# Kernel tuning notes

Hardware: AMD Instinct MI355X
Metric: run time of the kernel (lower is better)

Reference implementation:

```python
import jax, jax.numpy as jnp
import numpy as np

D_MODEL = 512
N_HEADS = 8
HEAD_DIM = D_MODEL // N_HEADS
BATCH = 4
SEQ = 2048


def setup_inputs() -> dict:
    key = jax.random.key(0)
    ks = jax.random.split(key, 9)
    s = 1.0 / np.sqrt(D_MODEL)
    inp = {
        "x": jax.random.normal(ks[0], (BATCH, SEQ, D_MODEL), dtype=jnp.float32),
        "wq": jax.random.uniform(ks[1], (D_MODEL, D_MODEL), jnp.float32, -s, s),
        "bq": jax.random.uniform(ks[2], (D_MODEL,), jnp.float32, -s, s),
        "wk": jax.random.uniform(ks[3], (D_MODEL, D_MODEL), jnp.float32, -s, s),
        "bk": jax.random.uniform(ks[4], (D_MODEL,), jnp.float32, -s, s),
        "wv": jax.random.uniform(ks[5], (D_MODEL, D_MODEL), jnp.float32, -s, s),
        "bv": jax.random.uniform(ks[6], (D_MODEL,), jnp.float32, -s, s),
        "wo": jax.random.uniform(ks[7], (D_MODEL, D_MODEL), jnp.float32, -s, s),
        "bo": jax.random.uniform(ks[8], (D_MODEL,), jnp.float32, -s, s),
    }
    return inp


def reference(x, wq, bq, wk, bk, wv, bv, wo, bo):
    B, S, D = x.shape
    H, Hd = N_HEADS, HEAD_DIM
    # projections (torch Linear: y = x @ W^T + b; here weights stored as [in, out])
    q = (x @ wq + bq).reshape(B, S, H, Hd).transpose(0, 2, 1, 3)  # [B,H,S,Hd]
    k = (x @ wk + bk).reshape(B, S, H, Hd).transpose(0, 2, 1, 3)
    v = (x @ wv + bv).reshape(B, S, H, Hd).transpose(0, 2, 1, 3)
    scores = jnp.einsum("bhqd,bhkd->bhqk", q, k) / jnp.sqrt(jnp.float32(Hd))
    attn = jax.nn.softmax(scores, axis=-1)
    o = jnp.einsum("bhqk,bhkd->bhqd", attn, v)  # [B,H,S,Hd]
    o = o.transpose(0, 2, 1, 3).reshape(B, S, D)
    return o @ wo + bo
```

## Files before the change

kernel.cpp:

```cpp
#include <hip/hip_runtime.h>
#include <math.h>

#define DM   512
#define SEQL 2048
#define NB   4
#define NH   8
#define HD   64

typedef _Float16 f16;
typedef _Float16 f16x4 __attribute__((ext_vector_type(4)));
typedef _Float16 f16x8 __attribute__((ext_vector_type(8)));
typedef float    f32x4 __attribute__((ext_vector_type(4)));

#define QSCALE 0.1803368801f
#define SOFTMAX_SHIFT 4.328085123f

typedef const __attribute__((address_space(1))) void* gp1_t;
typedef __attribute__((address_space(3))) void* lp3_t;
__device__ __forceinline__ void glds16(const void* g, void* l) {
    __builtin_amdgcn_global_load_lds((gp1_t)g, (lp3_t)l, 16, 0, 0);
}

__device__ __forceinline__ float fast_exp2(float x) {
#if __has_builtin(__builtin_amdgcn_exp2f)
    return __builtin_amdgcn_exp2f(x);
#else
    return exp2f(x);
#endif
}

__global__ __launch_bounds__(256) void prep_kernel(
    const float* __restrict__ x, f16* __restrict__ xh,
    const float* __restrict__ w0, const float* __restrict__ w1,
    const float* __restrict__ w2, const float* __restrict__ w3,
    f16* __restrict__ o0, f16* __restrict__ o1,
    f16* __restrict__ o2, f16* __restrict__ o3)
{
    __shared__ f16 t[64][72];
    const int bx = blockIdx.x;
    if (bx < 2048) {
        int i = (bx * 256 + threadIdx.x) * 8;
        float4 a = *(const float4*)&x[i];
        float4 b = *(const float4*)&x[i + 4];
        f16x8 h;
        h[0] = (f16)a.x; h[1] = (f16)a.y; h[2] = (f16)a.z; h[3] = (f16)a.w;
        h[4] = (f16)b.x; h[5] = (f16)b.y; h[6] = (f16)b.z; h[7] = (f16)b.w;
        *(f16x8*)&xh[i] = h;
        return;
    }
    const int idx  = bx - 2048;
    const int wsel = idx >> 6, tile = idx & 63;
    const float* w; f16* o;
    switch (wsel) {
        case 0:  w = w0; o = o0; break;
        case 1:  w = w1; o = o1; break;
        case 2:  w = w2; o = o2; break;
        default: w = w3; o = o3; break;
    }
    const int n0 = (tile & 7) * 64, k0 = (tile >> 3) * 64;
    const int tx = threadIdx.x & 63, tg = threadIdx.x >> 6;
    #pragma unroll
    for (int r = 0; r < 16; ++r) {
        int kl = tg * 16 + r;
        t[tx][kl] = (f16)w[(size_t)(k0 + kl) * DM + n0 + tx];
    }
    __syncthreads();
    #pragma unroll
    for (int r = 0; r < 16; ++r) {
        int nl = tg * 16 + r;
        o[(size_t)(n0 + nl) * DM + k0 + tx] = t[nl][tx];
    }
}

__global__ __launch_bounds__(256) void gemm_qkv(
    const f16* __restrict__ A, const f16* __restrict__ Wt,
    const float* __restrict__ bq, const float* __restrict__ bk,
    const float* __restrict__ bv,
    f16* __restrict__ qh, f16* __restrict__ kh, f16* __restrict__ vth)
{
    __shared__ f16 As[128 * 32];
    __shared__ f16 Bs[128 * 32];

    const int tid  = threadIdx.x;
    const int lane = tid & 63, wave = tid >> 6;
    const int quad = lane >> 4, l15 = lane & 15;
    const int wm = wave >> 1, wn = wave & 1;
    const int n0 = blockIdx.x * 128, m0 = blockIdx.y * 128;

    const int srow = wave * 32 + (lane >> 2);
    const int sk   = (lane & 3) * 8;

    f32x4 acc[4][4] = {};

    for (int k0 = 0; k0 < DM; k0 += 32) {
        glds16(&A [(size_t)(m0 + srow)      * DM + k0 + sk], &As[(wave * 32)      * 32]);
        glds16(&A [(size_t)(m0 + srow + 16) * DM + k0 + sk], &As[(wave * 32 + 16) * 32]);
        glds16(&Wt[(size_t)(n0 + srow)      * DM + k0 + sk], &Bs[(wave * 32)      * 32]);
        glds16(&Wt[(size_t)(n0 + srow + 16) * DM + k0 + sk], &Bs[(wave * 32 + 16) * 32]);
        __syncthreads();

        f16x8 af[4], bf[4];
        #pragma unroll
        for (int mt = 0; mt < 4; ++mt)
            af[mt] = *(f16x8*)&As[(wm * 64 + mt * 16 + l15) * 32 + quad * 8];
        #pragma unroll
        for (int nt = 0; nt < 4; ++nt)
            bf[nt] = *(f16x8*)&Bs[(wn * 64 + nt * 16 + l15) * 32 + quad * 8];
        #pragma unroll
        for (int mt = 0; mt < 4; ++mt)
            #pragma unroll
            for (int nt = 0; nt < 4; ++nt)
                acc[mt][nt] = __builtin_amdgcn_mfma_f32_16x16x32_f16(
                    af[mt], bf[nt], acc[mt][nt], 0, 0, 0);
        __syncthreads();
    }

    #pragma unroll
    for (int nt = 0; nt < 4; ++nt) {
        const int n   = n0 + wn * 64 + nt * 16 + l15;
        const int seg = n >> 9, nn = n & 511;
        const int h = nn >> 6, hd = nn & 63;
        const float bias = (seg == 0 ? bq : seg == 1 ? bk : bv)[nn];
        if (seg < 2) {
            f16* op = seg == 0 ? qh : kh;
            #pragma unroll
            for (int mt = 0; mt < 4; ++mt)
                #pragma unroll
                for (int rr = 0; rr < 4; ++rr) {
                    const int m = m0 + wm * 64 + mt * 16 + quad * 4 + rr;
                    const int bb = m >> 11, s = m & 2047;
                    op[(((size_t)(bb * NH + h) * SEQL + s) << 6) + hd] =
                        (f16)(acc[mt][nt][rr] + bias);
                }
        } else {
            #pragma unroll
            for (int mt = 0; mt < 4; ++mt) {
                const int mb = m0 + wm * 64 + mt * 16 + quad * 4;
                const int bb = mb >> 11, s = mb & 2047;
                f16x4 pk;
                #pragma unroll
                for (int rr = 0; rr < 4; ++rr) pk[rr] = (f16)(acc[mt][nt][rr] + bias);
                *(f16x4*)&vth[(((size_t)(bb * NH + h) * HD + hd) << 11) + s] = pk;
            }
        }
    }
}

__global__ __launch_bounds__(256) void gemm_out(
    const f16* __restrict__ A, const f16* __restrict__ Wt,
    const float* __restrict__ bias, float* __restrict__ out)
{
    __shared__ f16 As[128 * 32];
    __shared__ f16 Bs[128 * 32];

    const int tid  = threadIdx.x;
    const int lane = tid & 63, wave = tid >> 6;
    const int quad = lane >> 4, l15 = lane & 15;
    const int wm = wave >> 1, wn = wave & 1;
    const int n0 = blockIdx.x * 128, m0 = blockIdx.y * 128;

    const int srow = wave * 32 + (lane >> 2);
    const int sk   = (lane & 3) * 8;

    f32x4 acc[4][4] = {};

    for (int k0 = 0; k0 < DM; k0 += 32) {
        glds16(&A [(size_t)(m0 + srow)      * DM + k0 + sk], &As[(wave * 32)      * 32]);
        glds16(&A [(size_t)(m0 + srow + 16) * DM + k0 + sk], &As[(wave * 32 + 16) * 32]);
        glds16(&Wt[(size_t)(n0 + srow)      * DM + k0 + sk], &Bs[(wave * 32)      * 32]);
        glds16(&Wt[(size_t)(n0 + srow + 16) * DM + k0 + sk], &Bs[(wave * 32 + 16) * 32]);
        __syncthreads();

        f16x8 af[4], bf[4];
        #pragma unroll
        for (int mt = 0; mt < 4; ++mt)
            af[mt] = *(f16x8*)&As[(wm * 64 + mt * 16 + l15) * 32 + quad * 8];
        #pragma unroll
        for (int nt = 0; nt < 4; ++nt)
            bf[nt] = *(f16x8*)&Bs[(wn * 64 + nt * 16 + l15) * 32 + quad * 8];
        #pragma unroll
        for (int mt = 0; mt < 4; ++mt)
            #pragma unroll
            for (int nt = 0; nt < 4; ++nt)
                acc[mt][nt] = __builtin_amdgcn_mfma_f32_16x16x32_f16(
                    af[mt], bf[nt], acc[mt][nt], 0, 0, 0);
        __syncthreads();
    }

    #pragma unroll
    for (int nt = 0; nt < 4; ++nt) {
        const int n = n0 + wn * 64 + nt * 16 + l15;
        const float bv = bias[n];
        #pragma unroll
        for (int mt = 0; mt < 4; ++mt)
            #pragma unroll
            for (int rr = 0; rr < 4; ++rr) {
                const int m = m0 + wm * 64 + mt * 16 + quad * 4 + rr;
                out[(size_t)m * DM + n] = acc[mt][nt][rr] + bv;
            }
    }
}

__global__ __launch_bounds__(512) void flash_attn_mfma(
    const f16* __restrict__ Q, const f16* __restrict__ K,
    const f16* __restrict__ Vt, f16* __restrict__ O)
{
    __shared__ __align__(16) char smem[73728];
    f16*   Ks = (f16*)smem;
    f16*   Vs = (f16*)(smem + 18432);
    f16*   Ps = (f16*)(smem + 35840);
    float* Lx = (float*)(smem + 72704);
    float* cs = (float*)smem;

    const int tid  = threadIdx.x;
    const int lane = tid & 63, wave = tid >> 6;
    const int quad = lane >> 4, l15 = lane & 15;
    const int g  = wave >> 2;
    const int qg = wave & 3;
    const int bh = blockIdx.y, q0 = blockIdx.x * 128;
    const int b = bh >> 3, h = bh & 7;
    f16* Pw = Ps + wave * (32 * 72);

    const f16* Qb = Q  + (size_t)bh * SEQL * HD;
    const f16* Kb = K  + (size_t)bh * SEQL * HD;
    const f16* Vb = Vt + (size_t)bh * HD * SEQL;

    f16x8 qf[2][2];
    #pragma unroll
    for (int mq = 0; mq < 2; ++mq)
        #pragma unroll
        for (int ks = 0; ks < 2; ++ks) {
            qf[mq][ks] = *(const f16x8*)
                &Qb[(size_t)(q0 + qg * 32 + mq * 16 + l15) * HD + ks * 32 + quad * 8];
            #pragma unroll
            for (int j = 0; j < 8; ++j) qf[mq][ks][j] *= (f16)QSCALE;
        }

    const int krow = tid >> 3, kch = (tid & 7) * 8;
    const int vrow = tid >> 4, vch = (tid & 15) * 8;

    f16x8 kreg[2], vreg[2];
    #pragma unroll
    for (int r = 0; r < 2; ++r) {
        kreg[r] = *(const f16x8*)&Kb[(size_t)(krow + r * 64) * HD + kch];
        vreg[r] = *(const f16x8*)&Vb[(size_t)(vrow + r * 32) * SEQL + vch];
    }

    f32x4 o_acc[2][4] = {};
    float l_acc[2] = {0.f, 0.f};

    for (int kt = 0; kt < SEQL / 128; ++kt) {
        __syncthreads();
        #pragma unroll
        for (int r = 0; r < 2; ++r) {
            *(f16x8*)&Ks[(krow + r * 64) * 72 + kch]  = kreg[r];
            *(f16x8*)&Vs[(vrow + r * 32) * 136 + vch] = vreg[r];
        }
        __syncthreads();
        if (kt < SEQL / 128 - 1) {
            const int kb2 = (kt + 1) * 128;
            #pragma unroll
            for (int r = 0; r < 2; ++r) {
                kreg[r] = *(const f16x8*)&Kb[(size_t)(kb2 + krow + r * 64) * HD + kch];
                vreg[r] = *(const f16x8*)&Vb[(size_t)(vrow + r * 32) * SEQL + kb2 + vch];
            }
        }

        f32x4 sc[4][2];
        #pragma unroll
        for (int mk = 0; mk < 4; ++mk)
            #pragma unroll
            for (int mq = 0; mq < 2; ++mq)
                sc[mk][mq] = (f32x4){-SOFTMAX_SHIFT, -SOFTMAX_SHIFT,
                                     -SOFTMAX_SHIFT, -SOFTMAX_SHIFT};
        #pragma unroll
        for (int ks = 0; ks < 2; ++ks) {
            #pragma unroll
            for (int mk = 0; mk < 4; ++mk) {
                f16x8 af = *(f16x8*)&Ks[(g * 64 + mk * 16 + l15) * 72 + ks * 32 + quad * 8];
                #pragma unroll
                for (int mq = 0; mq < 2; ++mq)
                    sc[mk][mq] = __builtin_amdgcn_mfma_f32_16x16x32_f16(
                        af, qf[mq][ks], sc[mk][mq], 0, 0, 0);
            }
        }

        #pragma unroll
        for (int mk = 0; mk < 4; ++mk)
            #pragma unroll
            for (int mq = 0; mq < 2; ++mq) {
                float p0 = fast_exp2(sc[mk][mq][0]);
                float p1 = fast_exp2(sc[mk][mq][1]);
                float p2 = fast_exp2(sc[mk][mq][2]);
                float p3 = fast_exp2(sc[mk][mq][3]);
                l_acc[mq] += (p0 + p1) + (p2 + p3);
                f16x4 pk;
                pk[0] = (f16)p0; pk[1] = (f16)p1;
                pk[2] = (f16)p2; pk[3] = (f16)p3;
                *(f16x4*)&Pw[(mq * 16 + l15) * 72 + mk * 16 + quad * 4] = pk;
            }

        #pragma unroll
        for (int kc = 0; kc < 2; ++kc) {
            f16x8 pa0 = *(f16x8*)&Pw[(l15)      * 72 + kc * 32 + quad * 8];
            f16x8 pa1 = *(f16x8*)&Pw[(16 + l15) * 72 + kc * 32 + quad * 8];
            #pragma unroll
            for (int nt = 0; nt < 4; ++nt) {
                f16x8 vb = *(f16x8*)&Vs[(nt * 16 + l15) * 136 + g * 64 + kc * 32 + quad * 8];
                o_acc[0][nt] = __builtin_amdgcn_mfma_f32_16x16x32_f16(
                    pa0, vb, o_acc[0][nt], 0, 0, 0);
                o_acc[1][nt] = __builtin_amdgcn_mfma_f32_16x16x32_f16(
                    pa1, vb, o_acc[1][nt], 0, 0, 0);
            }
        }
    }

    #pragma unroll
    for (int mq = 0; mq < 2; ++mq) {
        float rs = l_acc[mq];
        rs += __shfl_xor(rs, 16);
        rs += __shfl_xor(rs, 32);
        l_acc[mq] = rs;
    }

    __syncthreads();
    if (quad == 0) {
        Lx[wave * 32 + l15]      = l_acc[0];
        Lx[wave * 32 + 16 + l15] = l_acc[1];
    }
    if (g == 1) {
        #pragma unroll
        for (int mq = 0; mq < 2; ++mq)
            #pragma unroll
            for (int r = 0; r < 4; ++r) {
                const int ql = mq * 16 + quad * 4 + r;
                #pragma unroll
                for (int nt = 0; nt < 4; ++nt)
                    cs[(qg * 32 + ql) * 68 + nt * 16 + l15] = o_acc[mq][nt][r];
            }
    }
    __syncthreads();
    if (g == 0) {
        #pragma unroll
        for (int mq = 0; mq < 2; ++mq)
            #pragma unroll
            for (int r = 0; r < 4; ++r) {
                const int ql = mq * 16 + quad * 4 + r;
                const float inv = 1.0f / (Lx[qg * 32 + ql] + Lx[(4 + qg) * 32 + ql]);
                const int s = q0 + qg * 32 + ql;
                #pragma unroll
                for (int nt = 0; nt < 4; ++nt) {
                    float ov = o_acc[mq][nt][r] + cs[(qg * 32 + ql) * 68 + nt * 16 + l15];
                    O[((size_t)(b * SEQL + s)) * DM + h * HD + nt * 16 + l15] =
                        (f16)(ov * inv);
                }
            }
    }
}

extern "C" void kernel_launch(void* const* d_in, const int* in_sizes, int n_in,
                              void* d_out, int out_size, void* d_ws, size_t ws_size,
                              hipStream_t stream) {
    const float* x  = (const float*)d_in[0];
    const float* wq = (const float*)d_in[1];
    const float* bq = (const float*)d_in[2];
    const float* wk = (const float*)d_in[3];
    const float* bk = (const float*)d_in[4];
    const float* wv = (const float*)d_in[5];
    const float* bv = (const float*)d_in[6];
    const float* wo = (const float*)d_in[7];
    const float* bo = (const float*)d_in[8];

    const size_t NE = (size_t)NB * SEQL * DM;
    const size_t WE = (size_t)DM * DM;
    f16* xh    = (f16*)d_ws;
    f16* wqkvt = xh + NE;
    f16* wot   = wqkvt + 3 * WE;
    f16* qh    = wot + WE;
    f16* kh    = qh + NE;
    f16* vth   = kh + NE;
    f16* oh    = vth + NE;

    prep_kernel<<<2304, 256, 0, stream>>>(
        x, xh, wq, wk, wv, wo,
        wqkvt, wqkvt + WE, wqkvt + 2 * WE, wot);

    gemm_qkv<<<dim3(12, 64), 256, 0, stream>>>(
        xh, wqkvt, bq, bk, bv, qh, kh, vth);

    flash_attn_mfma<<<dim3(SEQL / 128, NB * NH), 512, 0, stream>>>(qh, kh, vth, oh);

    gemm_out<<<dim3(4, 64), 256, 0, stream>>>(oh, wot, bo, (float*)d_out);
}
```

Measured before the change: 176.2 us.

## Vectorize GEMM epilogues via operand swap, retile out-proj, MFMA row sums in attention

The QKV GEMM swaps its MFMA operands for Q/K blocks so each lane holds four consecutive head-dim values, which lets the epilogue write packed f16x4 stores and load the bias as a vector. The output GEMM moves to 64x128 tiles with twice as many blocks, also swaps operands, and writes f32x4 vector stores. In flash attention the softmax row sums come from an extra MFMA against a ones vector instead of scalar adds and shuffles, and P is packed with cvt_pkrtz. The exp2 helper now calls exp2f, which may be slower than the raw builtin, and the extra MFMAs add matrix-unit work.

```diff
diff --git a/kernel.cpp b/kernel.cpp
--- a/kernel.cpp
+++ b/kernel.cpp
@@ -8,6 +8,7 @@
 #define HD   64
 
 typedef _Float16 f16;
+typedef __fp16   fp16x2 __attribute__((ext_vector_type(2)));
 typedef _Float16 f16x4 __attribute__((ext_vector_type(4)));
 typedef _Float16 f16x8 __attribute__((ext_vector_type(8)));
 typedef float    f32x4 __attribute__((ext_vector_type(4)));
@@ -21,13 +22,7 @@
     __builtin_amdgcn_global_load_lds((gp1_t)g, (lp3_t)l, 16, 0, 0);
 }
 
-__device__ __forceinline__ float fast_exp2(float x) {
-#if __has_builtin(__builtin_amdgcn_exp2f)
-    return __builtin_amdgcn_exp2f(x);
-#else
-    return exp2f(x);
-#endif
-}
+__device__ __forceinline__ float fast_exp2(float x) { return exp2f(x); }
 
 __global__ __launch_bounds__(256) void prep_kernel(
     const float* __restrict__ x, f16* __restrict__ xh,
@@ -86,6 +81,7 @@
     const int quad = lane >> 4, l15 = lane & 15;
     const int wm = wave >> 1, wn = wave & 1;
     const int n0 = blockIdx.x * 128, m0 = blockIdx.y * 128;
+    const bool qk = (blockIdx.x < 8);
 
     const int srow = wave * 32 + (lane >> 2);
     const int sk   = (lane & 3) * 8;
@@ -101,45 +97,63 @@
 
         f16x8 af[4], bf[4];
         #pragma unroll
-        for (int mt = 0; mt < 4; ++mt)
-            af[mt] = *(f16x8*)&As[(wm * 64 + mt * 16 + l15) * 32 + quad * 8];
-        #pragma unroll
-        for (int nt = 0; nt < 4; ++nt)
-            bf[nt] = *(f16x8*)&Bs[(wn * 64 + nt * 16 + l15) * 32 + quad * 8];
-        #pragma unroll
-        for (int mt = 0; mt < 4; ++mt)
-            #pragma unroll
-            for (int nt = 0; nt < 4; ++nt)
-                acc[mt][nt] = __builtin_amdgcn_mfma_f32_16x16x32_f16(
-                    af[mt], bf[nt], acc[mt][nt], 0, 0, 0);
-        __syncthreads();
-    }
-
-    #pragma unroll
-    for (int nt = 0; nt < 4; ++nt) {
-        const int n   = n0 + wn * 64 + nt * 16 + l15;
-        const int seg = n >> 9, nn = n & 511;
-        const int h = nn >> 6, hd = nn & 63;
-        const float bias = (seg == 0 ? bq : seg == 1 ? bk : bv)[nn];
-        if (seg < 2) {
-            f16* op = seg == 0 ? qh : kh;
-            #pragma unroll
-            for (int mt = 0; mt < 4; ++mt)
-                #pragma unroll
-                for (int rr = 0; rr < 4; ++rr) {
-                    const int m = m0 + wm * 64 + mt * 16 + quad * 4 + rr;
-                    const int bb = m >> 11, s = m & 2047;
-                    op[(((size_t)(bb * NH + h) * SEQL + s) << 6) + hd] =
-                        (f16)(acc[mt][nt][rr] + bias);
-                }
+        for (int i = 0; i < 4; ++i)
+            af[i] = *(f16x8*)&As[(wm * 64 + i * 16 + l15) * 32 + quad * 8];
+        #pragma unroll
+        for (int i = 0; i < 4; ++i)
+            bf[i] = *(f16x8*)&Bs[(wn * 64 + i * 16 + l15) * 32 + quad * 8];
+        if (qk) {
+            #pragma unroll
+            for (int i = 0; i < 4; ++i)
+                #pragma unroll
+                for (int j = 0; j < 4; ++j)
+                    acc[i][j] = __builtin_amdgcn_mfma_f32_16x16x32_f16(
+                        bf[i], af[j], acc[i][j], 0, 0, 0);
         } else {
             #pragma unroll
-            for (int mt = 0; mt < 4; ++mt) {
-                const int mb = m0 + wm * 64 + mt * 16 + quad * 4;
+            for (int i = 0; i < 4; ++i)
+                #pragma unroll
+                for (int j = 0; j < 4; ++j)
+                    acc[i][j] = __builtin_amdgcn_mfma_f32_16x16x32_f16(
+                        af[i], bf[j], acc[i][j], 0, 0, 0);
+        }
+        __syncthreads();
+    }
+
+    const int nwave = n0 + wn * 64;
+    const int seg   = nwave >> 9;
+    const int nn0   = nwave & 511;
+    const int h     = nn0 >> 6;
+
+    if (qk) {
+        f16* op = seg == 0 ? qh : kh;
+        const float* bp = seg == 0 ? bq : bk;
+        #pragma unroll
+        for (int i = 0; i < 4; ++i) {
+            const int hd = i * 16 + quad * 4;
+            f32x4 bv4 = *(const f32x4*)&bp[nn0 + hd];
+            #pragma unroll
+            for (int j = 0; j < 4; ++j) {
+                const int m = m0 + wm * 64 + j * 16 + l15;
+                const int bb = m >> 11, s = m & 2047;
+                f16x4 pk;
+                #pragma unroll
+                for (int rr = 0; rr < 4; ++rr) pk[rr] = (f16)(acc[i][j][rr] + bv4[rr]);
+                *(f16x4*)&op[(((size_t)(bb * NH + h) * SEQL + s) << 6) + hd] = pk;
+            }
+        }
+    } else {
+        #pragma unroll
+        for (int j = 0; j < 4; ++j) {
+            const int hd = j * 16 + l15;
+            const float bias = bv[nn0 + hd];
+            #pragma unroll
+            for (int i = 0; i < 4; ++i) {
+                const int mb = m0 + wm * 64 + i * 16 + quad * 4;
                 const int bb = mb >> 11, s = mb & 2047;
                 f16x4 pk;
                 #pragma unroll
-                for (int rr = 0; rr < 4; ++rr) pk[rr] = (f16)(acc[mt][nt][rr] + bias);
+                for (int rr = 0; rr < 4; ++rr) pk[rr] = (f16)(acc[i][j][rr] + bias);
                 *(f16x4*)&vth[(((size_t)(bb * NH + h) * HD + hd) << 11) + s] = pk;
             }
         }
@@ -150,54 +164,53 @@
     const f16* __restrict__ A, const f16* __restrict__ Wt,
     const float* __restrict__ bias, float* __restrict__ out)
 {
-    __shared__ f16 As[128 * 32];
+    __shared__ f16 As[64 * 32];
     __shared__ f16 Bs[128 * 32];
 
     const int tid  = threadIdx.x;
     const int lane = tid & 63, wave = tid >> 6;
     const int quad = lane >> 4, l15 = lane & 15;
-    const int wm = wave >> 1, wn = wave & 1;
-    const int n0 = blockIdx.x * 128, m0 = blockIdx.y * 128;
-
-    const int srow = wave * 32 + (lane >> 2);
-    const int sk   = (lane & 3) * 8;
-
-    f32x4 acc[4][4] = {};
+    const int wn = wave >> 1, wm = wave & 1;
+    const int n0 = blockIdx.x * 128, m0 = blockIdx.y * 64;
+
+    const int srowA = wave * 16 + (lane >> 2);
+    const int srowB = wave * 32 + (lane >> 2);
+    const int sk    = (lane & 3) * 8;
+
+    f32x4 acc[4][2] = {};
 
     for (int k0 = 0; k0 < DM; k0 += 32) {
-        glds16(&A [(size_t)(m0 + srow)      * DM + k0 + sk], &As[(wave * 32)      * 32]);
-        glds16(&A [(size_t)(m0 + srow + 16) * DM + k0 + sk], &As[(wave * 32 + 16) * 32]);
-        glds16(&Wt[(size_t)(n0 + srow)      * DM + k0 + sk], &Bs[(wave * 32)      * 32]);
-        glds16(&Wt[(size_t)(n0 + srow + 16) * DM + k0 + sk], &Bs[(wave * 32 + 16) * 32]);
-        __syncthreads();
-
-        f16x8 af[4], bf[4];
-        #pragma unroll
-        for (int mt = 0; mt < 4; ++mt)
-            af[mt] = *(f16x8*)&As[(wm * 64 + mt * 16 + l15) * 32 + quad * 8];
-        #pragma unroll
-        for (int nt = 0; nt < 4; ++nt)
-            bf[nt] = *(f16x8*)&Bs[(wn * 64 + nt * 16 + l15) * 32 + quad * 8];
-        #pragma unroll
-        for (int mt = 0; mt < 4; ++mt)
-            #pragma unroll
-            for (int nt = 0; nt < 4; ++nt)
-                acc[mt][nt] = __builtin_amdgcn_mfma_f32_16x16x32_f16(
-                    af[mt], bf[nt], acc[mt][nt], 0, 0, 0);
-        __syncthreads();
-    }
-
-    #pragma unroll
-    for (int nt = 0; nt < 4; ++nt) {
-        const int n = n0 + wn * 64 + nt * 16 + l15;
-        const float bv = bias[n];
-        #pragma unroll
-        for (int mt = 0; mt < 4; ++mt)
-            #pragma unroll
-            for (int rr = 0; rr < 4; ++rr) {
-                const int m = m0 + wm * 64 + mt * 16 + quad * 4 + rr;
-                out[(size_t)m * DM + n] = acc[mt][nt][rr] + bv;
-            }
+        glds16(&A [(size_t)(m0 + srowA)      * DM + k0 + sk], &As[(wave * 16)      * 32]);
+        glds16(&Wt[(size_t)(n0 + srowB)      * DM + k0 + sk], &Bs[(wave * 32)      * 32]);
+        glds16(&Wt[(size_t)(n0 + srowB + 16) * DM + k0 + sk], &Bs[(wave * 32 + 16) * 32]);
+        __syncthreads();
+
+        f16x8 af[4], bf[2];
+        #pragma unroll
+        for (int i = 0; i < 4; ++i)
+            af[i] = *(f16x8*)&Bs[(wn * 64 + i * 16 + l15) * 32 + quad * 8];
+        #pragma unroll
+        for (int j = 0; j < 2; ++j)
+            bf[j] = *(f16x8*)&As[(wm * 32 + j * 16 + l15) * 32 + quad * 8];
+        #pragma unroll
+        for (int i = 0; i < 4; ++i)
+            #pragma unroll
+            for (int j = 0; j < 2; ++j)
+                acc[i][j] = __builtin_amdgcn_mfma_f32_16x16x32_f16(
+                    af[i], bf[j], acc[i][j], 0, 0, 0);
+        __syncthreads();
+    }
+
+    #pragma unroll
+    for (int i = 0; i < 4; ++i) {
+        const int nb = n0 + wn * 64 + i * 16 + quad * 4;
+        f32x4 bv4 = *(const f32x4*)&bias[nb];
+        #pragma unroll
+        for (int j = 0; j < 2; ++j) {
+            const int m = m0 + wm * 32 + j * 16 + l15;
+            f32x4 val = acc[i][j] + bv4;
+            *(f32x4*)&out[(size_t)m * DM + nb] = val;
+        }
     }
 }
 
@@ -236,6 +249,10 @@
             for (int j = 0; j < 8; ++j) qf[mq][ks][j] *= (f16)QSCALE;
         }
 
+    f16x8 onesf;
+    #pragma unroll
+    for (int j = 0; j < 8; ++j) onesf[j] = (f16)1.0f;
+
     const int krow = tid >> 3, kch = (tid & 7) * 8;
     const int vrow = tid >> 4, vch = (tid & 15) * 8;
 
@@ -247,7 +264,7 @@
     }
 
     f32x4 o_acc[2][4] = {};
-    float l_acc[2] = {0.f, 0.f};
+    f32x4 o_l[2] = {};
 
     for (int kt = 0; kt < SEQL / 128; ++kt) {
         __syncthreads();
@@ -293,17 +310,18 @@
                 float p1 = fast_exp2(sc[mk][mq][1]);
                 float p2 = fast_exp2(sc[mk][mq][2]);
                 float p3 = fast_exp2(sc[mk][mq][3]);
-                l_acc[mq] += (p0 + p1) + (p2 + p3);
-                f16x4 pk;
-                pk[0] = (f16)p0; pk[1] = (f16)p1;
-                pk[2] = (f16)p2; pk[3] = (f16)p3;
-                *(f16x4*)&Pw[(mq * 16 + l15) * 72 + mk * 16 + quad * 4] = pk;
+                union { f16x4 v4; fp16x2 v2[2]; } pk;
+                pk.v2[0] = __builtin_amdgcn_cvt_pkrtz(p0, p1);
+                pk.v2[1] = __builtin_amdgcn_cvt_pkrtz(p2, p3);
+                *(f16x4*)&Pw[(mq * 16 + l15) * 72 + mk * 16 + quad * 4] = pk.v4;
             }
 
         #pragma unroll
         for (int kc = 0; kc < 2; ++kc) {
             f16x8 pa0 = *(f16x8*)&Pw[(l15)      * 72 + kc * 32 + quad * 8];
             f16x8 pa1 = *(f16x8*)&Pw[(16 + l15) * 72 + kc * 32 + quad * 8];
+            o_l[0] = __builtin_amdgcn_mfma_f32_16x16x32_f16(pa0, onesf, o_l[0], 0, 0, 0);
+            o_l[1] = __builtin_amdgcn_mfma_f32_16x16x32_f16(pa1, onesf, o_l[1], 0, 0, 0);
             #pragma unroll
             for (int nt = 0; nt < 4; ++nt) {
                 f16x8 vb = *(f16x8*)&Vs[(nt * 16 + l15) * 136 + g * 64 + kc * 32 + quad * 8];
@@ -315,18 +333,13 @@
         }
     }
 
-    #pragma unroll
-    for (int mq = 0; mq < 2; ++mq) {
-        float rs = l_acc[mq];
-        rs += __shfl_xor(rs, 16);
-        rs += __shfl_xor(rs, 32);
-        l_acc[mq] = rs;
-    }
-
     __syncthreads();
-    if (quad == 0) {
-        Lx[wave * 32 + l15]      = l_acc[0];
-        Lx[wave * 32 + 16 + l15] = l_acc[1];
+    if (l15 == 0) {
+        #pragma unroll
+        for (int mq = 0; mq < 2; ++mq)
+            #pragma unroll
+            for (int r = 0; r < 4; ++r)
+                Lx[wave * 32 + mq * 16 + quad * 4 + r] = o_l[mq][r];
     }
     if (g == 1) {
         #pragma unroll
@@ -390,5 +403,5 @@
 
     flash_attn_mfma<<<dim3(SEQL / 128, NB * NH), 512, 0, stream>>>(qh, kh, vth, oh);
 
-    gemm_out<<<dim3(4, 64), 256, 0, stream>>>(oh, wot, bo, (float*)d_out);
-}
+    gemm_out<<<dim3(4, 128), 256, 0, stream>>>(oh, wot, bo, (float*)d_out);
+}
```

Result: slower. 195.7 us (+11.1%).
